# Performance work log

Measured on AMD Instinct MI355X. Metric: run time of the kernel, lower is better.

## Reference

```python
import jax, jax.numpy as jnp
import numpy as np

N = 50000      # total nodes
E = 800000     # total edges
G = 1000       # graphs in batch
H = 128        # in_channels == hidden_channels
L = 3          # num GCN layers
C = 6          # num classes
EPS = 1e-5     # BatchNorm eps


def setup_inputs() -> dict:
    key = jax.random.key(0)
    ks = jax.random.split(key, 8)
    x = jax.random.normal(ks[0], (N, H), jnp.float32)
    edge_index = jax.random.randint(ks[1], (2, E), 0, N)
    batch = jnp.sort(jax.random.randint(ks[2], (N,), 0, G))
    conv_w = jax.random.normal(ks[3], (L, H, H), jnp.float32) * 0.05
    conv_b = jnp.zeros((L, H), jnp.float32)
    bn_g = jnp.ones((L, H), jnp.float32)
    bn_b = jnp.zeros((L, H), jnp.float32)
    mlp_w1 = jax.random.normal(ks[4], (H, H), jnp.float32) * 0.05
    mlp_b1 = jnp.zeros((H,), jnp.float32)
    mlp_w2 = jax.random.normal(ks[5], (H, C), jnp.float32) * 0.05
    mlp_b2 = jnp.zeros((C,), jnp.float32)
    return {"x": x, "edge_index": edge_index, "batch": batch,
            "conv_w": conv_w, "conv_b": conv_b, "bn_g": bn_g, "bn_b": bn_b,
            "mlp_w1": mlp_w1, "mlp_b1": mlp_b1, "mlp_w2": mlp_w2, "mlp_b2": mlp_b2}


def reference(x, edge_index, batch, conv_w, conv_b, bn_g, bn_b, mlp_w1, mlp_b1, mlp_w2, mlp_b2):
    src, dst = edge_index[0], edge_index[1]
    # GCN symmetric norm with self-loops: deg over A+I
    deg = jax.ops.segment_sum(jnp.ones((E,), x.dtype), dst, num_segments=N) + 1.0
    dis = jax.lax.rsqrt(deg)                      # deg^{-1/2}, [N]
    edge_norm = (dis[src] * dis[dst])[:, None]    # [E,1]
    self_norm = (dis * dis)[:, None]              # [N,1] self-loop weight 1/deg

    for l in range(L):
        h = x @ conv_w[l]                                             # [N,H]
        agg = jax.ops.segment_sum(h[src] * edge_norm, dst, num_segments=N)
        h = agg + h * self_norm + conv_b[l]
        # BatchNorm (training-mode batch statistics, biased var)
        mu = jnp.mean(h, axis=0)
        var = jnp.var(h, axis=0)
        hn = (h - mu) * jax.lax.rsqrt(var + EPS)
        x = jax.nn.relu(hn * bn_g[l] + bn_b[l])   # dropout = identity (eval)

    # global mean pool per graph
    sums = jax.ops.segment_sum(x, batch, num_segments=G)              # [G,H]
    cnt = jax.ops.segment_sum(jnp.ones((N,), x.dtype), batch, num_segments=G)
    pooled = sums / jnp.maximum(cnt, 1.0)[:, None]

    h = jax.nn.relu(pooled @ mlp_w1 + mlp_b1)
    return h @ mlp_w2 + mlp_b2                                         # [G,C]
```

## Files before the change

### kernel.cpp

```cpp
#include <hip/hip_runtime.h>

#define Nn 50000
#define Ee 800000
#define Gg 1000
#define Hh 128
#define Cc 6
#define EPSf 1e-5f
#define SB 1024
#define NSB ((Nn + SB - 1) / SB)

typedef unsigned short u16;
typedef unsigned int u32;
typedef __attribute__((ext_vector_type(8))) short bf16x8;
typedef __attribute__((ext_vector_type(4))) float f32x4;

static __device__ inline u16 f2bf(float f) {
    u32 u = __float_as_uint(f);
    u32 r = (u + 0x7fffu + ((u >> 16) & 1u)) >> 16;
    return (u16)r;
}
static __device__ inline float bf_lo(u32 v) { return __uint_as_float(v << 16); }
static __device__ inline float bf_hi(u32 v) { return __uint_as_float(v & 0xffff0000u); }
static __device__ inline u32 pack2(float a, float b) {
    return ((u32)f2bf(b) << 16) | (u32)f2bf(a);
}

__global__ __launch_bounds__(256) void k_pre(const float* __restrict__ W3,
                                             u16* __restrict__ WT3,
                                             int* __restrict__ indeg,
                                             float* __restrict__ stats3) {
    int t = blockIdx.x * blockDim.x + threadIdx.x;
    if (t < Nn) indeg[t] = 0;
    if (t < 3 * 2 * Hh) stats3[t] = 0.0f;

    if (blockIdx.x < 3) {
        __shared__ u16 tbuf[Hh * 136];
        int l = blockIdx.x;
        const float* W = W3 + l * Hh * Hh;
        u16* WT = WT3 + l * Hh * Hh;
        int tid = threadIdx.x;
#pragma unroll
        for (int i = 0; i < 16; i++) {
            int v = tid + 256 * i;
            int r = v >> 5, c4 = v & 31;
            float4 d = ((const float4*)W)[v];
            u16* p = tbuf + r * 136 + c4 * 4;
            p[0] = f2bf(d.x); p[1] = f2bf(d.y); p[2] = f2bf(d.z); p[3] = f2bf(d.w);
        }
        __syncthreads();
#pragma unroll
        for (int i = 0; i < 64; i++) {
            int o = tid + 256 * i;
            int n = o >> 7, k = o & 127;
            WT[o] = tbuf[k * 136 + n];
        }
    }
}

__global__ __launch_bounds__(256) void k_scan1(const int* __restrict__ indeg,
                                               int* __restrict__ rs,
                                               int* __restrict__ bsum,
                                               float* __restrict__ dis,
                                               const int* __restrict__ batch,
                                               int* __restrict__ gstart) {
    __shared__ int ts[256];
    int b = blockIdx.x;
    int t = threadIdx.x;
    int base = b * SB + t * 4;
    int v[4] = {0, 0, 0, 0};
#pragma unroll
    for (int j = 0; j < 4; j++) {
        int i = base + j;
        if (i < Nn) { v[j] = indeg[i]; dis[i] = rsqrtf((float)v[j] + 1.0f); }
    }
    int g = b * 256 + t;
    if (g <= Gg) {
        int lo = 0, hi = Nn;
        while (lo < hi) {
            int mid = (lo + hi) >> 1;
            if (batch[mid] < g) lo = mid + 1; else hi = mid;
        }
        gstart[g] = lo;
    }
    int tsum = v[0] + v[1] + v[2] + v[3];
    ts[t] = tsum;
    __syncthreads();
    for (int off = 1; off < 256; off <<= 1) {
        int x = (t >= off) ? ts[t - off] : 0;
        __syncthreads();
        ts[t] += x;
        __syncthreads();
    }
    int run = (t == 0) ? 0 : ts[t - 1];
    if (t == 255) bsum[b] = ts[255];
#pragma unroll
    for (int j = 0; j < 4; j++) {
        int i = base + j;
        if (i < Nn) { rs[i] = run; run += v[j]; }
    }
}

__global__ __launch_bounds__(256) void k_scan2(int* __restrict__ rs,
                                               const int* __restrict__ bsum) {
    __shared__ int lboff[NSB];
    int t = threadIdx.x;
    if (t < 64) {
        int orig = (t < NSB) ? bsum[t] : 0;
        int v = orig;
#pragma unroll
        for (int off = 1; off < 64; off <<= 1) {
            int u = __shfl_up(v, off, 64);
            if (t >= off) v += u;
        }
        if (t < NSB) lboff[t] = v - orig;
    }
    __syncthreads();
    int i = blockIdx.x * blockDim.x + t;
    if (i < Nn) rs[i] += lboff[i >> 10];
    if (blockIdx.x == 0 && t == 0) rs[Nn] = Ee;
}

__global__ void k_fill(const int* __restrict__ ei, const int* __restrict__ rs,
                       const u16* __restrict__ rank,
                       const float* __restrict__ dis, u32* __restrict__ recs) {
    int e = blockIdx.x * blockDim.x + threadIdx.x;
    if (e >= Ee) return;
    int s = ei[e];
    int d = ei[Ee + e];
    int slot = rs[d] + (int)rank[e];
    float w = dis[s] * dis[d];
    recs[slot] = ((u32)f2bf(w) << 16) | (u32)s;
}

__global__ __launch_bounds__(256) void k_gemm(const u16* __restrict__ Xin,
                                              const float* __restrict__ Xf,
                                              const u16* __restrict__ WT,
                                              u16* __restrict__ Yh,
                                              const float* __restrict__ stats,
                                              const float* __restrict__ gam,
                                              const float* __restrict__ bet,
                                              int mode,
                                              const int* __restrict__ ei,
                                              int* __restrict__ indeg,
                                              u16* __restrict__ rank) {
    __shared__ u16 wt[Hh * 136];
    __shared__ float s_scale[Hh], s_shift[Hh];
    int tid = threadIdx.x;

    if (mode == 2) {
        int g = blockIdx.x * 256 + tid;
        int e0 = g * 4;
        if (e0 < Ee) {
            int4 d4 = ((const int4*)(ei + Ee))[g];
            ushort4 r4;
            r4.x = (u16)atomicAdd(&indeg[d4.x], 1);
            r4.y = (u16)atomicAdd(&indeg[d4.y], 1);
            r4.z = (u16)atomicAdd(&indeg[d4.z], 1);
            r4.w = (u16)atomicAdd(&indeg[d4.w], 1);
            ((ushort4*)rank)[g] = r4;
        }
    }

    if (mode == 1 && tid < Hh) {
        float mu = stats[tid] * (1.0f / Nn);
        float var = stats[Hh + tid] * (1.0f / Nn) - mu * mu;
        float sc = rsqrtf(var + EPSf) * gam[tid];
        s_scale[tid] = sc;
        s_shift[tid] = bet[tid] - mu * sc;
    }
#pragma unroll
    for (int i = 0; i < 8; i++) {
        int v = tid + 256 * i;
        int n = v >> 4, k8 = v & 15;
        uint4 d = ((const uint4*)WT)[v];
        *((uint4*)(wt + n * 136 + k8 * 8)) = d;
    }
    __syncthreads();

    int wv = tid >> 6, lane = tid & 63;
    int m = lane & 15, q = lane >> 4;
    int row0 = blockIdx.x * 64 + wv * 16;
    int lrow = row0 + m;
    if (lrow >= Nn) lrow = Nn - 1;
    const u16* xrow = Xin + lrow * Hh + q * 8;
    const float* xfrow = Xf + lrow * Hh + q * 8;

    f32x4 acc[8] = {};
#pragma unroll
    for (int k0 = 0; k0 < Hh; k0 += 32) {
        bf16x8 a;
        if (mode == 1) {
            int cb = k0 + q * 8;
            uint4 p = *(const uint4*)(xrow + k0);
            float4 sc0 = *(const float4*)(s_scale + cb);
            float4 sc1 = *(const float4*)(s_scale + cb + 4);
            float4 sh0 = *(const float4*)(s_shift + cb);
            float4 sh1 = *(const float4*)(s_shift + cb + 4);
            float f0 = fmaxf(bf_lo(p.x) * sc0.x + sh0.x, 0.0f);
            float f1 = fmaxf(bf_hi(p.x) * sc0.y + sh0.y, 0.0f);
            float f2 = fmaxf(bf_lo(p.y) * sc0.z + sh0.z, 0.0f);
            float f3 = fmaxf(bf_hi(p.y) * sc0.w + sh0.w, 0.0f);
            float f4 = fmaxf(bf_lo(p.z) * sc1.x + sh1.x, 0.0f);
            float f5 = fmaxf(bf_hi(p.z) * sc1.y + sh1.y, 0.0f);
            float f6 = fmaxf(bf_lo(p.w) * sc1.z + sh1.z, 0.0f);
            float f7 = fmaxf(bf_hi(p.w) * sc1.w + sh1.w, 0.0f);
            union { bf16x8 v; u32 u[4]; } cv;
            cv.u[0] = pack2(f0, f1);
            cv.u[1] = pack2(f2, f3);
            cv.u[2] = pack2(f4, f5);
            cv.u[3] = pack2(f6, f7);
            a = cv.v;
        } else if (mode == 2) {
            float4 u0 = *(const float4*)(xfrow + k0);
            float4 u1 = *(const float4*)(xfrow + k0 + 4);
            union { bf16x8 v; u32 u[4]; } cv;
            cv.u[0] = pack2(u0.x, u0.y);
            cv.u[1] = pack2(u0.z, u0.w);
            cv.u[2] = pack2(u1.x, u1.y);
            cv.u[3] = pack2(u1.z, u1.w);
            a = cv.v;
        } else {
            a = *(const bf16x8*)(xrow + k0);
        }
#pragma unroll
        for (int t = 0; t < 8; t++) {
            bf16x8 b = *(const bf16x8*)(wt + (t * 16 + m) * 136 + k0 + q * 8);
            acc[t] = __builtin_amdgcn_mfma_f32_16x16x32_bf16(a, b, acc[t], 0, 0, 0);
        }
    }

    int orow0 = row0 + q * 4;
#pragma unroll
    for (int t = 0; t < 8; t++) {
#pragma unroll
        for (int r = 0; r < 4; r++) {
            int rr = orow0 + r;
            if (rr < Nn) Yh[rr * Hh + t * 16 + m] = f2bf(acc[t][r]);
        }
    }
}

__global__ __launch_bounds__(256) void k_gather(const u16* __restrict__ Yh,
                                                const float* __restrict__ dis,
                                                const float* __restrict__ bias,
                                                const int* __restrict__ rs,
                                                const u32* __restrict__ recs,
                                                u16* __restrict__ Ah) {
    int node = blockIdx.x * 4 + (threadIdx.x >> 6);
    if (node >= Nn) return;
    int lane = threadIdx.x & 63;

    const u32* rows = (const u32*)Yh;
    float dn = dis[node];
    u32 hv = rows[node * 64 + lane];
    float2 bv = ((const float2*)bias)[lane];
    float sn = dn * dn;
    float2 acc;
    acc.x = bf_lo(hv) * sn + bv.x;
    acc.y = bf_hi(hv) * sn + bv.y;

    int beg = rs[node];
    int end = rs[node + 1];

    for (int base = beg; base < end; base += 64) {
        int me = base + lane;
        u32 myrec = recs[me < end ? me : end - 1];
        int cnt = end - base;
        if (cnt > 64) cnt = 64;
        for (int i0 = 0; i0 < cnt; i0 += 16) {
            u32 rec[16]; float wgt[16]; u32 val[16];
#pragma unroll
            for (int i = 0; i < 16; i++) {
                int si = i0 + i;
                int sc = si < cnt ? si : cnt - 1;
                rec[i] = __shfl(myrec, sc, 64);
                wgt[i] = (si < cnt) ? __uint_as_float(rec[i] & 0xffff0000u) : 0.0f;
            }
#pragma unroll
            for (int i = 0; i < 16; i++) val[i] = rows[(rec[i] & 0xffffu) * 64 + lane];
#pragma unroll
            for (int i = 0; i < 16; i++) {
                acc.x += bf_lo(val[i]) * wgt[i];
                acc.y += bf_hi(val[i]) * wgt[i];
            }
        }
    }
    __builtin_nontemporal_store(pack2(acc.x, acc.y), (u32*)Ah + node * 64 + lane);
}

__global__ __launch_bounds__(256) void k_stats(const u16* __restrict__ Ah,
                                               float* __restrict__ stats) {
    __shared__ float sh[4][256];
    int t = threadIdx.x;
    int jc = t & 63, ro = t >> 6;
    const u32* col = (const u32*)Ah + jc;
    float sx = 0.f, sy = 0.f, qx = 0.f, qy = 0.f;
    for (int r = blockIdx.x * 16 + ro * 4; r < Nn; r += 4096) {
        u32 v[4];
#pragma unroll
        for (int k = 0; k < 4; k++) {
            int rr = r + k;
            v[k] = (rr < Nn) ? col[rr * 64] : 0u;
        }
#pragma unroll
        for (int k = 0; k < 4; k++) {
            float a = bf_lo(v[k]), b = bf_hi(v[k]);
            sx += a; sy += b; qx += a * a; qy += b * b;
        }
    }
    sh[0][t] = sx; sh[1][t] = sy; sh[2][t] = qx; sh[3][t] = qy;
    __syncthreads();
    if (t < 64) {
        sx = sh[0][t] + sh[0][t + 64] + sh[0][t + 128] + sh[0][t + 192];
        sy = sh[1][t] + sh[1][t + 64] + sh[1][t + 128] + sh[1][t + 192];
        qx = sh[2][t] + sh[2][t + 64] + sh[2][t + 128] + sh[2][t + 192];
        qy = sh[3][t] + sh[3][t + 64] + sh[3][t + 128] + sh[3][t + 192];
        atomicAdd(&stats[2 * t], sx);
        atomicAdd(&stats[2 * t + 1], sy);
        atomicAdd(&stats[Hh + 2 * t], qx);
        atomicAdd(&stats[Hh + 2 * t + 1], qy);
    }
}

__global__ __launch_bounds__(128) void k_poolmlp(const u16* __restrict__ Ah,
                                                 const float* __restrict__ stats,
                                                 const float* __restrict__ gam,
                                                 const float* __restrict__ bet,
                                                 const int* __restrict__ gstart,
                                                 const float* __restrict__ W1,
                                                 const float* __restrict__ b1,
                                                 const float* __restrict__ W2,
                                                 const float* __restrict__ b2,
                                                 float* __restrict__ out) {
    int g = blockIdx.x;
    int c = threadIdx.x;
    __shared__ float p[Hh];
    __shared__ float hid[Hh];
    float mu = stats[c] * (1.0f / Nn);
    float var = stats[Hh + c] * (1.0f / Nn) - mu * mu;
    float sc = rsqrtf(var + EPSf) * gam[c];
    float sf = bet[c] - mu * sc;
    int s = gstart[g], e = gstart[g + 1];
    float sum0 = 0.0f, sum1 = 0.0f;
    int r = s;
    for (; r + 1 < e; r += 2) {
        float v0 = __uint_as_float((u32)Ah[r * Hh + c] << 16);
        float v1 = __uint_as_float((u32)Ah[(r + 1) * Hh + c] << 16);
        sum0 += fmaxf(v0 * sc + sf, 0.0f);
        sum1 += fmaxf(v1 * sc + sf, 0.0f);
    }
    if (r < e) {
        float v = __uint_as_float((u32)Ah[r * Hh + c] << 16);
        sum0 += fmaxf(v * sc + sf, 0.0f);
    }
    int n = e - s;
    p[c] = (sum0 + sum1) / (float)(n > 1 ? n : 1);
    __syncthreads();
    float acc = b1[c];
    for (int k = 0; k < Hh; k++) acc += p[k] * W1[k * Hh + c];
    hid[c] = fmaxf(acc, 0.0f);
    __syncthreads();
    if (c < Cc) {
        float acc2 = b2[c];
        for (int k = 0; k < Hh; k++) acc2 += hid[k] * W2[k * Cc + c];
        out[g * Cc + c] = acc2;
    }
}

extern "C" void kernel_launch(void* const* d_in, const int* in_sizes, int n_in,
                              void* d_out, int out_size, void* d_ws, size_t ws_size,
                              hipStream_t stream) {
    const float* x      = (const float*)d_in[0];
    const int*   ei     = (const int*)d_in[1];
    const int*   batch  = (const int*)d_in[2];
    const float* conv_w = (const float*)d_in[3];
    const float* conv_b = (const float*)d_in[4];
    const float* bn_g   = (const float*)d_in[5];
    const float* bn_b   = (const float*)d_in[6];
    const float* w1     = (const float*)d_in[7];
    const float* b1     = (const float*)d_in[8];
    const float* w2     = (const float*)d_in[9];
    const float* b2     = (const float*)d_in[10];
    float* out = (float*)d_out;

    u16*   Yh      = (u16*)d_ws;
    u16*   Ah      = Yh + Nn * Hh;
    u16*   WT      = Ah + Nn * Hh;
    float* dis     = (float*)(WT + 3 * Hh * Hh);
    float* stats3  = dis + Nn;
    int*   indeg   = (int*)(stats3 + 3 * 2 * Hh);
    int*   rs      = indeg + Nn;
    int*   gstart  = rs + Nn + 1;
    int*   bsum    = gstart + Gg + 1;
    u32*   recs    = (u32*)(bsum + NSB);
    u16*   rank    = (u16*)(recs + Ee);

    k_pre<<<(Nn + 255) / 256, 256, 0, stream>>>(conv_w, WT, indeg, stats3);
    k_gemm<<<(Nn + 63) / 64, 256, 0, stream>>>(nullptr, x, WT, Yh,
                                               nullptr, nullptr, nullptr, 2,
                                               ei, indeg, rank);
    k_scan1<<<NSB, 256, 0, stream>>>(indeg, rs, bsum, dis, batch, gstart);
    k_scan2<<<(Nn + 255) / 256, 256, 0, stream>>>(rs, bsum);
    k_fill<<<(Ee + 255) / 256, 256, 0, stream>>>(ei, rs, rank, dis, recs);

    for (int l = 0; l < 3; l++) {
        k_gather<<<(Nn + 3) / 4, 256, 0, stream>>>(Yh, dis, conv_b + l * Hh, rs,
                                                   recs, Ah);
        k_stats<<<256, 256, 0, stream>>>(Ah, stats3 + l * 2 * Hh);
        if (l < 2) {
            k_gemm<<<(Nn + 63) / 64, 256, 0, stream>>>(Ah, nullptr,
                                                       WT + (l + 1) * Hh * Hh, Yh,
                                                       stats3 + l * 2 * Hh,
                                                       bn_g + l * Hh, bn_b + l * Hh, 1,
                                                       nullptr, nullptr, nullptr);
        }
    }

    k_poolmlp<<<Gg, 128, 0, stream>>>(Ah, stats3 + 2 * 2 * Hh, bn_g + 2 * Hh,
                                      bn_b + 2 * Hh, gstart, w1, b1, w2, b2, out);
}
```

Measured before the change: 354.6 us.

## Replace global-atomic in-degree counting with per-block LDS histograms and merge

Global atomicAdd on the in-degree array, formerly fused into the first GEMM, is replaced by a two-stage scheme. 64 blocks each build a shared-memory histogram over their edge slice, packing two 16-bit counters per word and processing the node range in two halves. A merge kernel then prefix-sums the per-block partials to produce base offsets and in-degrees, and the fill kernel combines local rank with the block base offset. This removes contention on global atomics but adds two launches, a 64×25000-word partials buffer, and only 64 blocks for the histogram, each scanning its edge slice twice.

After: 340.3 us. 4.0% less time.

```diff
diff --git a/kernel.cpp b/kernel.cpp
--- a/kernel.cpp
+++ b/kernel.cpp
@@ -8,6 +8,10 @@
 #define EPSf 1e-5f
 #define SB 1024
 #define NSB ((Nn + SB - 1) / SB)
+#define NBH 64
+#define EPB (Ee / NBH)
+#define NW (Nn / 2)
+#define HWH (NW / 2)
 
 typedef unsigned short u16;
 typedef unsigned int u32;
@@ -27,34 +31,71 @@
 
 __global__ __launch_bounds__(256) void k_pre(const float* __restrict__ W3,
                                              u16* __restrict__ WT3,
-                                             int* __restrict__ indeg,
                                              float* __restrict__ stats3) {
     int t = blockIdx.x * blockDim.x + threadIdx.x;
-    if (t < Nn) indeg[t] = 0;
     if (t < 3 * 2 * Hh) stats3[t] = 0.0f;
 
-    if (blockIdx.x < 3) {
-        __shared__ u16 tbuf[Hh * 136];
-        int l = blockIdx.x;
-        const float* W = W3 + l * Hh * Hh;
-        u16* WT = WT3 + l * Hh * Hh;
-        int tid = threadIdx.x;
-#pragma unroll
-        for (int i = 0; i < 16; i++) {
-            int v = tid + 256 * i;
-            int r = v >> 5, c4 = v & 31;
-            float4 d = ((const float4*)W)[v];
-            u16* p = tbuf + r * 136 + c4 * 4;
-            p[0] = f2bf(d.x); p[1] = f2bf(d.y); p[2] = f2bf(d.z); p[3] = f2bf(d.w);
-        }
+    __shared__ u16 tbuf[Hh * 136];
+    int l = blockIdx.x;
+    const float* W = W3 + l * Hh * Hh;
+    u16* WT = WT3 + l * Hh * Hh;
+    int tid = threadIdx.x;
+#pragma unroll
+    for (int i = 0; i < 16; i++) {
+        int v = tid + 256 * i;
+        int r = v >> 5, c4 = v & 31;
+        float4 d = ((const float4*)W)[v];
+        u16* p = tbuf + r * 136 + c4 * 4;
+        p[0] = f2bf(d.x); p[1] = f2bf(d.y); p[2] = f2bf(d.z); p[3] = f2bf(d.w);
+    }
+    __syncthreads();
+#pragma unroll
+    for (int i = 0; i < 64; i++) {
+        int o = tid + 256 * i;
+        int n = o >> 7, k = o & 127;
+        WT[o] = tbuf[k * 136 + n];
+    }
+}
+
+__global__ __launch_bounds__(1024) void k_hist(const int* __restrict__ ei_dst,
+                                               u16* __restrict__ rankL,
+                                               u32* __restrict__ partials) {
+    __shared__ u32 h[HWH];
+    int b = blockIdx.x, t = threadIdx.x;
+    int e0 = b * EPB;
+    u32* P = partials + b * NW;
+#pragma unroll 1
+    for (int half = 0; half < 2; half++) {
+        int wlo = half * HWH;
+        for (int i = t; i < HWH; i += 1024) h[i] = 0u;
         __syncthreads();
-#pragma unroll
-        for (int i = 0; i < 64; i++) {
-            int o = tid + 256 * i;
-            int n = o >> 7, k = o & 127;
-            WT[o] = tbuf[k * 136 + n];
-        }
-    }
+        for (int i = t; i < EPB; i += 1024) {
+            int d = ei_dst[e0 + i];
+            int w = d >> 1;
+            if (w >= wlo && w < wlo + HWH) {
+                u32 old = atomicAdd(&h[w - wlo], (d & 1) ? 65536u : 1u);
+                rankL[e0 + i] = (u16)((d & 1) ? (old >> 16) : (old & 0xffffu));
+            }
+        }
+        __syncthreads();
+        for (int i = t; i < HWH; i += 1024) P[wlo + i] = h[i];
+        __syncthreads();
+    }
+}
+
+__global__ __launch_bounds__(256) void k_merge(const u32* __restrict__ partials,
+                                               u32* __restrict__ base_off,
+                                               int* __restrict__ indeg) {
+    int w = blockIdx.x * 256 + threadIdx.x;
+    if (w >= NW) return;
+    u32 run = 0;
+#pragma unroll 8
+    for (int b = 0; b < NBH; b++) {
+        u32 v = partials[b * NW + w];
+        base_off[b * NW + w] = run;
+        run += v;
+    }
+    ((int2*)indeg)[w] = make_int2((int)(run & 0xffffu), (int)(run >> 16));
 }
 
 __global__ __launch_bounds__(256) void k_scan1(const int* __restrict__ indeg,
@@ -121,13 +162,17 @@
 }
 
 __global__ void k_fill(const int* __restrict__ ei, const int* __restrict__ rs,
-                       const u16* __restrict__ rank,
+                       const u16* __restrict__ rankL,
+                       const u32* __restrict__ base_off,
                        const float* __restrict__ dis, u32* __restrict__ recs) {
     int e = blockIdx.x * blockDim.x + threadIdx.x;
     if (e >= Ee) return;
     int s = ei[e];
     int d = ei[Ee + e];
-    int slot = rs[d] + (int)rank[e];
+    int blk = e / EPB;
+    u32 bo = base_off[blk * NW + (d >> 1)];
+    int rank = (int)rankL[e] + (int)((d & 1) ? (bo >> 16) : (bo & 0xffffu));
+    int slot = rs[d] + rank;
     float w = dis[s] * dis[d];
     recs[slot] = ((u32)f2bf(w) << 16) | (u32)s;
 }
@@ -139,27 +184,10 @@
                                               const float* __restrict__ stats,
                                               const float* __restrict__ gam,
                                               const float* __restrict__ bet,
-                                              int mode,
-                                              const int* __restrict__ ei,
-                                              int* __restrict__ indeg,
-                                              u16* __restrict__ rank) {
+                                              int mode) {
     __shared__ u16 wt[Hh * 136];
     __shared__ float s_scale[Hh], s_shift[Hh];
     int tid = threadIdx.x;
-
-    if (mode == 2) {
-        int g = blockIdx.x * 256 + tid;
-        int e0 = g * 4;
-        if (e0 < Ee) {
-            int4 d4 = ((const int4*)(ei + Ee))[g];
-            ushort4 r4;
-            r4.x = (u16)atomicAdd(&indeg[d4.x], 1);
-            r4.y = (u16)atomicAdd(&indeg[d4.y], 1);
-            r4.z = (u16)atomicAdd(&indeg[d4.z], 1);
-            r4.w = (u16)atomicAdd(&indeg[d4.w], 1);
-            ((ushort4*)rank)[g] = r4;
-        }
-    }
 
     if (mode == 1 && tid < Hh) {
         float mu = stats[tid] * (1.0f / Nn);
@@ -210,7 +238,7 @@
             cv.u[2] = pack2(f4, f5);
             cv.u[3] = pack2(f6, f7);
             a = cv.v;
-        } else if (mode == 2) {
+        } else {
             float4 u0 = *(const float4*)(xfrow + k0);
             float4 u1 = *(const float4*)(xfrow + k0 + 4);
             union { bf16x8 v; u32 u[4]; } cv;
@@ -219,8 +247,6 @@
             cv.u[2] = pack2(u1.x, u1.y);
             cv.u[3] = pack2(u1.z, u1.w);
             a = cv.v;
-        } else {
-            a = *(const bf16x8*)(xrow + k0);
         }
 #pragma unroll
         for (int t = 0; t < 8; t++) {
@@ -393,15 +419,18 @@
     int*   gstart  = rs + Nn + 1;
     int*   bsum    = gstart + Gg + 1;
     u32*   recs    = (u32*)(bsum + NSB);
-    u16*   rank    = (u16*)(recs + Ee);
-
-    k_pre<<<(Nn + 255) / 256, 256, 0, stream>>>(conv_w, WT, indeg, stats3);
+    u16*   rankL   = (u16*)(recs + Ee);
+    u32*   partials = (u32*)(rankL + Ee);
+    u32*   base_off = partials + NBH * NW;
+
+    k_pre<<<3, 256, 0, stream>>>(conv_w, WT, stats3);
     k_gemm<<<(Nn + 63) / 64, 256, 0, stream>>>(nullptr, x, WT, Yh,
-                                               nullptr, nullptr, nullptr, 2,
-                                               ei, indeg, rank);
+                                               nullptr, nullptr, nullptr, 2);
+    k_hist<<<NBH, 1024, 0, stream>>>(ei + Ee, rankL, partials);
+    k_merge<<<(NW + 255) / 256, 256, 0, stream>>>(partials, base_off, indeg);
     k_scan1<<<NSB, 256, 0, stream>>>(indeg, rs, bsum, dis, batch, gstart);
     k_scan2<<<(Nn + 255) / 256, 256, 0, stream>>>(rs, bsum);
-    k_fill<<<(Ee + 255) / 256, 256, 0, stream>>>(ei, rs, rank, dis, recs);
+    k_fill<<<(Ee + 255) / 256, 256, 0, stream>>>(ei, rs, rankL, base_off, dis, recs);
 
     for (int l = 0; l < 3; l++) {
         k_gather<<<(Nn + 3) / 4, 256, 0, stream>>>(Yh, dis, conv_b + l * Hh, rs,
@@ -411,8 +440,7 @@
             k_gemm<<<(Nn + 63) / 64, 256, 0, stream>>>(Ah, nullptr,
                                                        WT + (l + 1) * Hh * Hh, Yh,
                                                        stats3 + l * 2 * Hh,
-                                                       bn_g + l * Hh, bn_b + l * Hh, 1,
-                                                       nullptr, nullptr, nullptr);
+                                                       bn_g + l * Hh, bn_b + l * Hh, 1);
         }
     }
 
```
